# Kernel optimization log

Hardware: AMD Instinct MI355X
Metric: run time of the kernel (lower is better)

Reference implementation:

```python
import jax, jax.numpy as jnp
from jax import lax
import numpy as np

N = 4096      # graph nodes
K = 16        # sampled local-neighborhood size (2-hop proxy)
T = 16        # number of templates
NT = 16       # nodes per template
D = 128       # node feature dim
OUTER = 3     # proximal / mirror-descent iterations
INNER = 5     # sinkhorn iterations per outer step
EPS_REL = 0.1 # entropic reg relative to cost range
TINY = 1e-16


def setup_inputs() -> dict:
    key = jax.random.key(0)
    ks = jax.random.split(key, 8)
    x = jax.random.normal(ks[0], (N, D), jnp.float32)
    adj = (jax.random.uniform(ks[1], (N, N)) < 0.004).astype(jnp.float32)
    adj = jnp.maximum(adj, adj.T)
    neighbors = jax.random.randint(ks[2], (N, K), 0, N, dtype=jnp.int32)
    templates = (jax.random.randint(ks[3], (T, NT, NT), 0, 2).astype(jnp.float32)
                 + 0.01 * jax.random.normal(ks[4], (T, NT, NT), jnp.float32))
    templates_features = 0.0012 + 0.02 * jax.random.normal(ks[5], (T, NT, D), jnp.float32)
    q0 = jax.random.uniform(ks[6], (T, NT), jnp.float32)
    alpha0 = jnp.zeros((1,), jnp.float32)
    return {"x": x, "adj": adj, "neighbors": neighbors, "templates": templates,
            "templates_features": templates_features, "q0": q0, "alpha0": alpha0}


def _ltfgw(x, adj, neighbors, templates, templates_features, q0, alpha0):
    n, d = x.shape
    t, nt, _ = templates.shape
    k1 = neighbors.shape[1] + 1
    nb = jnp.concatenate([jnp.arange(n, dtype=neighbors.dtype)[:, None], neighbors], axis=1)  # [N,K1]
    Fi = x[nb]                                    # [N,K1,D] local node features
    C1 = adj[nb[:, :, None], nb[:, None, :]]      # [N,K1,K1] local structure
    C2 = templates                                # [T,NT,NT]
    alpha = jax.nn.sigmoid(alpha0[0])
    q = jax.nn.softmax(q0, axis=1)                # [T,NT] template node weights
    p = jnp.full((k1,), 1.0 / k1, x.dtype)        # uniform local weights
    # squared-euclidean feature cost M: [N,T,K1,NT]
    M = (jnp.sum(Fi**2, -1)[:, None, :, None]
         + jnp.sum(templates_features**2, -1)[None, :, None, :]
         - 2.0 * jnp.einsum('nkd,tmd->ntkm', Fi, templates_features))
    # constant part of squared-loss GW cost
    cC = (jnp.einsum('nij,j->ni', C1**2, p)[:, None, :, None]
          + jnp.einsum('tm,tlm->tl', q, C2**2)[None, :, None, :])
    G0 = jnp.broadcast_to(p[None, None, :, None] * q[None, :, None, :], (n, t, k1, nt))

    def outer_step(G, _):
        gw_grad = cC - 2.0 * jnp.einsum('nij,ntjm,tlm->ntil', C1, G, C2)
        grad = (1.0 - alpha) * M + alpha * gw_grad
        lo = jnp.min(grad, axis=(-2, -1), keepdims=True)
        hi = jnp.max(grad, axis=(-2, -1), keepdims=True)
        eps = EPS_REL * (hi - lo) + TINY
        Kmat = jnp.exp(-(grad - lo) / eps)        # per-(n,t) shift leaves plan invariant

        def sink(uv, _):
            u, v = uv
            u = p[None, None, :] / jnp.maximum(jnp.einsum('ntkm,ntm->ntk', Kmat, v), TINY)
            v = q[None] / jnp.maximum(jnp.einsum('ntkm,ntk->ntm', Kmat, u), TINY)
            return (u, v), None

        u0 = jnp.ones((n, t, k1), x.dtype)
        v0 = jnp.ones((n, t, nt), x.dtype)
        (u, v), _ = lax.scan(sink, (u0, v0), None, length=INNER)
        return u[..., None] * Kmat * v[..., None, :], None

    G, _ = lax.scan(outer_step, G0, None, length=OUTER)
    gw = cC - 2.0 * jnp.einsum('nij,ntjm,tlm->ntil', C1, G, C2)
    # fused GW distance of every node's local graph to every template: [N,T]
    return jnp.sum(((1.0 - alpha) * M + alpha * gw) * G, axis=(-2, -1))


def reference(x, adj, neighbors, templates, templates_features, q0, alpha0):
    return _ltfgw(x, adj, neighbors, templates, templates_features, q0, alpha0)
```

## Files before the change

### kernel.cpp

```cpp
#include <hip/hip_runtime.h>
#include <math.h>


#define NN 4096
#define KNB 16
#define K1 17
#define TSTR 296
#define TINYF 1e-16f

typedef const __attribute__((address_space(4))) float* c4fp;
typedef const __attribute__((address_space(4))) int*   c4ip;
__device__ __forceinline__ float sload(const float* p){ return *(c4fp)(unsigned long long)p; }
__device__ __forceinline__ int   sloadi(const int* p) { return *(c4ip)(unsigned long long)p; }

template<int CTRL>
__device__ __forceinline__ float dppmov(float x) {
  return __int_as_float(
      __builtin_amdgcn_update_dpp(0, __float_as_int(x), CTRL, 0xF, 0xF, true));
}
__device__ __forceinline__ float xor4v(float x) {
  return dppmov<0x1B>(dppmov<0x141>(x));
}
__device__ __forceinline__ float rsum16(float x) {
  x += dppmov<0xB1>(x); x += dppmov<0x4E>(x);
  x += xor4v(x);        x += dppmov<0x128>(x);
  return x;
}
__device__ __forceinline__ float rmin16(float x) {
  x = fminf(x, dppmov<0xB1>(x)); x = fminf(x, dppmov<0x4E>(x));
  x = fminf(x, xor4v(x));        x = fminf(x, dppmov<0x128>(x));
  return x;
}
__device__ __forceinline__ float rmax16(float x) {
  x = fmaxf(x, dppmov<0xB1>(x)); x = fmaxf(x, dppmov<0x4E>(x));
  x = fmaxf(x, xor4v(x));        x = fmaxf(x, dppmov<0x128>(x));
  return x;
}
__device__ __forceinline__ float rcpn(float x) {
  float r = __builtin_amdgcn_rcpf(x);
  return r * (2.f - x * r);
}

#define WSTEP(C, R) { g = dppmov<C>(g); acc = fmaf(g, c2reg[R], acc); }
#define WALK15() \
  WSTEP(0xB1,1)  WSTEP(0x1B,2)  WSTEP(0xB1,3)  WSTEP(0x141,4) \
  WSTEP(0xB1,5)  WSTEP(0x1B,6)  WSTEP(0xB1,7)  WSTEP(0x140,8) \
  WSTEP(0xB1,9)  WSTEP(0x1B,10) WSTEP(0xB1,11) WSTEP(0x141,12) \
  WSTEP(0xB1,13) WSTEP(0x1B,14) WSTEP(0xB1,15)

#define PG_GEMM  512
#define PG_PACK  (PG_GEMM + 1024)
#define PG_XSQ   (PG_PACK + 1024)
#define PG_SCAL  PG_XSQ
#define PG_TOT   (PG_SCAL + 1)

__global__ __launch_bounds__(256) void prep_combined(
    const float* __restrict__ x, const float* __restrict__ adj,
    const float* __restrict__ templates_, const float* __restrict__ tf,
    const float* __restrict__ q0, const float* __restrict__ alpha0,
    float* __restrict__ P, unsigned long long* __restrict__ pk,
    float* __restrict__ xsq, float* __restrict__ tfsq,
    float* __restrict__ qmat, float* __restrict__ cq,
    float* __restrict__ walpha) {
  __shared__ __align__(16) float smem[2 * 64 * 68];
  const int b = blockIdx.x, tid = threadIdx.x;

  if (b < PG_GEMM) {
    float (*As)[68] = (float (*)[68])smem;
    float (*Bs)[68] = (float (*)[68])(smem + 64*68);
    int tx = tid & 15, ty = tid >> 4;
    int r0 = (b & 127) * 32, c0 = (b >> 7) * 64;
    float acc[2][4] = {};
    for (int h = 0; h < 2; ++h) {
      __syncthreads();
#pragma unroll
      for (int q = 0; q < 2; ++q) {
        int f = tid + 256*q;
        int row = f >> 4, d4 = (f & 15) << 2;
        float4 a = *(const float4*)&x[(r0+row)*128 + h*64 + d4];
        As[d4+0][row]=a.x; As[d4+1][row]=a.y; As[d4+2][row]=a.z; As[d4+3][row]=a.w;
      }
#pragma unroll
      for (int q = 0; q < 4; ++q) {
        int f = tid + 256*q;
        int col = f >> 4, d4 = (f & 15) << 2;
        float4 bb = *(const float4*)&tf[(c0+col)*128 + h*64 + d4];
        Bs[d4+0][col]=bb.x; Bs[d4+1][col]=bb.y; Bs[d4+2][col]=bb.z; Bs[d4+3][col]=bb.w;
      }
      __syncthreads();
#pragma unroll
      for (int d = 0; d < 64; ++d) {
        float2 a = *(const float2*)&As[d][ty*2];
        float4 bb = *(const float4*)&Bs[d][tx*4];
        float av[2]={a.x,a.y}, bv[4]={bb.x,bb.y,bb.z,bb.w};
#pragma unroll
        for (int i = 0; i < 2; ++i)
#pragma unroll
          for (int j = 0; j < 4; ++j) acc[i][j] = fmaf(av[i], bv[j], acc[i][j]);
      }
    }
#pragma unroll
    for (int i = 0; i < 2; ++i) {
      float4 o; o.x=acc[i][0]; o.y=acc[i][1]; o.z=acc[i][2]; o.w=acc[i][3];
      *(float4*)&P[(r0 + ty*2 + i)*256 + c0 + tx*4] = o;
    }
    return;
  }

  if (b < PG_PACK) {
    int wave = (b - PG_GEMM)*4 + (tid >> 6);
    int lane = tid & 63;
#pragma unroll 4
    for (int it = 0; it < 64; ++it) {
      int w64 = wave + it*4096;
      float v = adj[(size_t)w64*64 + lane];
      unsigned long long m = __ballot(v != 0.f);
      if (lane == 0) pk[w64] = m;
    }
    return;
  }

  if (b < PG_XSQ) {
    int n = (b - PG_PACK)*4 + (tid >> 6), lane = tid & 63;
    float2 v = *(const float2*)&x[n*128 + lane*2];
    float s = fmaf(v.x, v.x, v.y*v.y);
    s += __shfl_xor(s,1); s += __shfl_xor(s,2);  s += __shfl_xor(s,4);
    s += __shfl_xor(s,8); s += __shfl_xor(s,16); s += __shfl_xor(s,32);
    if (lane == 0) xsq[n] = s;
    return;
  }

  {
    int t = tid >> 4, l = tid & 15;
    if (tid == 0) walpha[0] = 1.f / (1.f + expf(-alpha0[0]));
    float qr[16]; float mx = -3.0e38f;
#pragma unroll
    for (int m = 0; m < 16; ++m) { qr[m] = q0[t*16+m]; mx = fmaxf(mx, qr[m]); }
    float s = 0.f;
#pragma unroll
    for (int m = 0; m < 16; ++m) { qr[m] = expf(qr[m]-mx); s += qr[m]; }
    float inv = 1.f / s;
    qmat[tid] = qr[l] * inv;
    float c = 0.f;
#pragma unroll
    for (int m = 0; m < 16; ++m) {
      float c2 = templates_[t*256 + l*16 + m];
      c = fmaf(qr[m]*inv, c2*c2, c);
    }
    cq[tid] = c;
    float ts = 0.f;
#pragma unroll
    for (int dq = 0; dq < 32; ++dq) {
      float4 v = *(const float4*)&tf[tid*128 + dq*4];
      ts = fmaf(v.x,v.x,ts); ts = fmaf(v.y,v.y,ts);
      ts = fmaf(v.z,v.z,ts); ts = fmaf(v.w,v.w,ts);
    }
    tfsq[tid] = ts;
  }
}

__global__ __launch_bounds__(256, 2) void ltfgw_main(
    const float* __restrict__ P, const unsigned* __restrict__ pku,
    const float* __restrict__ xsq, const float* __restrict__ tfsq,
    const float* __restrict__ qmat, const float* __restrict__ cq,
    const float* __restrict__ walpha, const int* __restrict__ neighbors,
    const float* __restrict__ templates_, float* __restrict__ out) {
  __shared__ __align__(16) float Ksh[16 * TSTR];
  __shared__ __align__(16) float Ush[256];
  __shared__ __align__(16) float Vsh[256];
  __shared__ int rowm[20];

  const int tid = threadIdx.x;
  const int t = tid >> 4, l = tid & 15;
  const int n = blockIdx.x;

  const float alpha = sload(walpha);
  const float oma = 1.f - alpha;
  const float na2 = -2.f * alpha;

  int nbk[K1];
  nbk[0] = n;
#pragma unroll
  for (int k = 1; k < K1; ++k) nbk[k] = sloadi(neighbors + n*KNB + (k-1));

  if (tid < K1) {
    int row = (tid == 0) ? n : neighbors[n*KNB + tid - 1];
    const unsigned* prow = pku + row*128;
    unsigned m = 0;
#pragma unroll
    for (int j = 0; j < K1; ++j) {
      int col = nbk[j];
      unsigned w = prow[col >> 5];
      m |= ((w >> (col & 31)) & 1u) << j;
    }
    rowm[tid] = (int)m;
  }
  __syncthreads();
  int rmv[K1];
#pragma unroll
  for (int i = 0; i < K1; ++i) rmv[i] = rowm[i];

  const float tfsq_l = tfsq[tid];
  const float cq_l   = cq[tid];
  const float q_l    = qmat[tid];

  float Mcol[K1];
#pragma unroll
  for (int k = 0; k < K1; ++k) {
    float xs  = sload(xsq + nbk[k]);
    float cc1 = (float)__popc((unsigned)rmv[k]) * (1.f/17.f);
    float pv  = P[nbk[k]*256 + tid];
    Mcol[k] = oma * (xs + tfsq_l - 2.f*pv) + alpha * (cc1 + cq_l);
  }

  float c2reg[16];
#pragma unroll
  for (int r = 0; r < 16; ++r)
    c2reg[r] = na2 * templates_[t*256 + l*16 + (l ^ r)];

  float Gcol[K1];
#pragma unroll
  for (int j = 0; j < K1; ++j) Gcol[j] = (1.f/17.f) * q_l;

  const int tb = t * TSTR;
  float ur[16], u16 = 0.f, vm = 1.f;

#pragma unroll 1
  for (int outer = 0; outer < 3; ++outer) {
    float Kc[K1];
    float lo = 3.0e38f, hi = -3.0e38f;
#pragma unroll
    for (int i = 0; i < K1; ++i) {
      float gr = Mcol[i];
      int rmi = __builtin_amdgcn_readfirstlane(rmv[i]);
      if (rmi) {
        float s = 0.f;
#pragma unroll
        for (int j = 0; j < K1; ++j)
          if (rmi & (1 << j)) s += Gcol[j];
        float g = s, acc = s * c2reg[0];
        WALK15()
        gr += acc;
      }
      Kc[i] = gr;
      lo = fminf(lo, gr); hi = fmaxf(hi, gr);
    }
    lo = rmin16(lo); hi = rmax16(hi);
    float eps = 0.1f * (hi - lo) + TINYF;
    float sc = 1.4426950408889634f * __builtin_amdgcn_rcpf(eps);
#pragma unroll
    for (int i = 0; i < K1; ++i) {
      Kc[i] = __builtin_amdgcn_exp2f((lo - Kc[i]) * sc);
      Ksh[tb + i*17 + l] = Kc[i];
    }
    float Krow[16];
#pragma unroll
    for (int jq = 0; jq < 4; ++jq) {
      float4 v = *(const float4*)&Ksh[tb + l*17 + jq*4];
      Krow[jq*4+0]=v.x; Krow[jq*4+1]=v.y; Krow[jq*4+2]=v.z; Krow[jq*4+3]=v.w;
    }

    float vlane = 1.f;
    Vsh[tid] = 1.f;
#pragma unroll 1
    for (int it = 0; it < 5; ++it) {
      float vr[16];
#pragma unroll
      for (int q = 0; q < 4; ++q) {
        float4 v = *(const float4*)&Vsh[t*16 + q*4];
        vr[q*4+0]=v.x; vr[q*4+1]=v.y; vr[q*4+2]=v.z; vr[q*4+3]=v.w;
      }
      float w = 0.f;
#pragma unroll
      for (int j = 0; j < 16; ++j) w = fmaf(Krow[j], vr[j], w);
      float w16 = rsum16(Kc[16] * vlane);
      float um = (1.f/17.f) * rcpn(fmaxf(w,   TINYF));
      u16      = (1.f/17.f) * rcpn(fmaxf(w16, TINYF));
      Ush[tid] = um;
#pragma unroll
      for (int q = 0; q < 4; ++q) {
        float4 v = *(const float4*)&Ush[t*16 + q*4];
        ur[q*4+0]=v.x; ur[q*4+1]=v.y; ur[q*4+2]=v.z; ur[q*4+3]=v.w;
      }
      float sg = u16 * Kc[16];
#pragma unroll
      for (int k = 0; k < 16; ++k) sg = fmaf(ur[k], Kc[k], sg);
      vlane = q_l * rcpn(fmaxf(sg, TINYF));
      Vsh[tid] = vlane;
    }
    vm = vlane;
#pragma unroll
    for (int k = 0; k < 16; ++k) Gcol[k] = ur[k] * Kc[k] * vm;
    Gcol[16] = u16 * Kc[16] * vm;
  }

  float acc1 = 0.f;
#pragma unroll
  for (int i = 0; i < K1; ++i) acc1 = fmaf(Mcol[i], Gcol[i], acc1);
#pragma unroll
  for (int i = 0; i < K1; ++i) {
    int rmi = __builtin_amdgcn_readfirstlane(rmv[i]);
    if (rmi) {
      float s = 0.f;
#pragma unroll
      for (int j = 0; j < K1; ++j)
        if (rmi & (1 << j)) s += Gcol[j];
      float g = s, acc = s * c2reg[0];
      WALK15()
      acc1 = fmaf(acc, Gcol[i], acc1);
    }
  }
  float accout = rsum16(acc1);
  if (l == 0) out[n*16 + t] = accout;
}

extern "C" void kernel_launch(void* const* d_in, const int* in_sizes, int n_in,
                              void* d_out, int out_size, void* d_ws, size_t ws_size,
                              hipStream_t stream) {
  const float* x          = (const float*)d_in[0];
  const float* adj        = (const float*)d_in[1];
  const int*   neighbors  = (const int*)  d_in[2];
  const float* templates_ = (const float*)d_in[3];
  const float* tfeat      = (const float*)d_in[4];
  const float* q0         = (const float*)d_in[5];
  const float* alpha0     = (const float*)d_in[6];
  float* out = (float*)d_out;

  float* ws     = (float*)d_ws;
  float* P      = ws;
  float* xsq    = P + 4096*256;
  float* tfsq   = xsq + 4096;
  float* qmat   = tfsq + 256;
  float* cq     = qmat + 256;
  float* walpha = cq + 256;
  unsigned long long* pk = (unsigned long long*)(walpha + 8);

  hipLaunchKernelGGL(prep_combined, dim3(PG_TOT), dim3(256), 0, stream,
                     x, adj, templates_, tfeat, q0, alpha0,
                     P, pk, xsq, tfsq, qmat, cq, walpha);
  hipLaunchKernelGGL(ltfgw_main, dim3(4096), dim3(256), 0, stream,
                     P, (const unsigned*)pk, xsq, tfsq, qmat, cq, walpha,
                     neighbors, templates_, out);
}
```

Before: 195.4 us.

## Gather local adjacency bitmasks in prep kernel instead of packing full adjacency

The prep kernel no longer ballot-packs the whole 4096x4096 adjacency matrix into bits. Instead it gathers only the 17x17 local-structure entries per node directly from adj and writes per-node row bitmasks, which the main kernel reads as scalar loads. This drops a full 64MB adjacency read and removes a syncthreads plus the shared-memory handoff in the main kernel. Launch bounds are raised to 4 blocks per SIMD, which may force register spilling. Only 17 of every 64 lanes do the scattered gathers, so that part runs at low efficiency.

```diff
diff --git a/kernel.cpp b/kernel.cpp
--- a/kernel.cpp
+++ b/kernel.cpp
@@ -6,6 +6,7 @@
 #define KNB 16
 #define K1 17
 #define TSTR 296
+#define RBITS_STR 32
 #define TINYF 1e-16f
 
 typedef const __attribute__((address_space(4))) float* c4fp;
@@ -49,16 +50,17 @@
   WSTEP(0xB1,13) WSTEP(0x1B,14) WSTEP(0xB1,15)
 
 #define PG_GEMM  512
-#define PG_PACK  (PG_GEMM + 1024)
-#define PG_XSQ   (PG_PACK + 1024)
+#define PG_BITS  (PG_GEMM + 1024)
+#define PG_XSQ   (PG_BITS + 1024)
 #define PG_SCAL  PG_XSQ
 #define PG_TOT   (PG_SCAL + 1)
 
 __global__ __launch_bounds__(256) void prep_combined(
     const float* __restrict__ x, const float* __restrict__ adj,
-    const float* __restrict__ templates_, const float* __restrict__ tf,
-    const float* __restrict__ q0, const float* __restrict__ alpha0,
-    float* __restrict__ P, unsigned long long* __restrict__ pk,
+    const int* __restrict__ neighbors, const float* __restrict__ templates_,
+    const float* __restrict__ tf, const float* __restrict__ q0,
+    const float* __restrict__ alpha0,
+    float* __restrict__ P, int* __restrict__ rowbits,
     float* __restrict__ xsq, float* __restrict__ tfsq,
     float* __restrict__ qmat, float* __restrict__ cq,
     float* __restrict__ walpha) {
@@ -107,21 +109,28 @@
     return;
   }
 
-  if (b < PG_PACK) {
-    int wave = (b - PG_GEMM)*4 + (tid >> 6);
-    int lane = tid & 63;
-#pragma unroll 4
-    for (int it = 0; it < 64; ++it) {
-      int w64 = wave + it*4096;
-      float v = adj[(size_t)w64*64 + lane];
-      unsigned long long m = __ballot(v != 0.f);
-      if (lane == 0) pk[w64] = m;
+  if (b < PG_BITS) {
+    int g = b - PG_GEMM;
+    int sub = tid >> 6;
+    int row = tid & 63;
+    int n = g*4 + sub;
+    if (row < K1) {
+      int nbs[K1];
+      nbs[0] = n;
+#pragma unroll
+      for (int k = 1; k < K1; ++k) nbs[k] = neighbors[n*KNB + k - 1];
+      const float* arow = adj + (size_t)nbs[row]*NN;
+      unsigned m = 0;
+#pragma unroll
+      for (int j = 0; j < K1; ++j)
+        m |= (arow[nbs[j]] != 0.f ? 1u : 0u) << j;
+      rowbits[n*RBITS_STR + row] = (int)m;
     }
     return;
   }
 
   if (b < PG_XSQ) {
-    int n = (b - PG_PACK)*4 + (tid >> 6), lane = tid & 63;
+    int n = (b - PG_BITS)*4 + (tid >> 6), lane = tid & 63;
     float2 v = *(const float2*)&x[n*128 + lane*2];
     float s = fmaf(v.x, v.x, v.y*v.y);
     s += __shfl_xor(s,1); s += __shfl_xor(s,2);  s += __shfl_xor(s,4);
@@ -159,8 +168,8 @@
   }
 }
 
-__global__ __launch_bounds__(256, 2) void ltfgw_main(
-    const float* __restrict__ P, const unsigned* __restrict__ pku,
+__global__ __launch_bounds__(256, 4) void ltfgw_main(
+    const float* __restrict__ P, const int* __restrict__ rowbits,
     const float* __restrict__ xsq, const float* __restrict__ tfsq,
     const float* __restrict__ qmat, const float* __restrict__ cq,
     const float* __restrict__ walpha, const int* __restrict__ neighbors,
@@ -168,7 +177,6 @@
   __shared__ __align__(16) float Ksh[16 * TSTR];
   __shared__ __align__(16) float Ush[256];
   __shared__ __align__(16) float Vsh[256];
-  __shared__ int rowm[20];
 
   const int tid = threadIdx.x;
   const int t = tid >> 4, l = tid & 15;
@@ -183,22 +191,9 @@
 #pragma unroll
   for (int k = 1; k < K1; ++k) nbk[k] = sloadi(neighbors + n*KNB + (k-1));
 
-  if (tid < K1) {
-    int row = (tid == 0) ? n : neighbors[n*KNB + tid - 1];
-    const unsigned* prow = pku + row*128;
-    unsigned m = 0;
-#pragma unroll
-    for (int j = 0; j < K1; ++j) {
-      int col = nbk[j];
-      unsigned w = prow[col >> 5];
-      m |= ((w >> (col & 31)) & 1u) << j;
-    }
-    rowm[tid] = (int)m;
-  }
-  __syncthreads();
   int rmv[K1];
 #pragma unroll
-  for (int i = 0; i < K1; ++i) rmv[i] = rowm[i];
+  for (int i = 0; i < K1; ++i) rmv[i] = sloadi(rowbits + n*RBITS_STR + i);
 
   const float tfsq_l = tfsq[tid];
   const float cq_l   = cq[tid];
@@ -232,7 +227,7 @@
 #pragma unroll
     for (int i = 0; i < K1; ++i) {
       float gr = Mcol[i];
-      int rmi = __builtin_amdgcn_readfirstlane(rmv[i]);
+      int rmi = rmv[i];
       if (rmi) {
         float s = 0.f;
 #pragma unroll
@@ -299,7 +294,7 @@
   for (int i = 0; i < K1; ++i) acc1 = fmaf(Mcol[i], Gcol[i], acc1);
 #pragma unroll
   for (int i = 0; i < K1; ++i) {
-    int rmi = __builtin_amdgcn_readfirstlane(rmv[i]);
+    int rmi = rmv[i];
     if (rmi) {
       float s = 0.f;
 #pragma unroll
@@ -333,12 +328,12 @@
   float* qmat   = tfsq + 256;
   float* cq     = qmat + 256;
   float* walpha = cq + 256;
-  unsigned long long* pk = (unsigned long long*)(walpha + 8);
+  int*   rowbits= (int*)(walpha + 8);
 
   hipLaunchKernelGGL(prep_combined, dim3(PG_TOT), dim3(256), 0, stream,
-                     x, adj, templates_, tfeat, q0, alpha0,
-                     P, pk, xsq, tfsq, qmat, cq, walpha);
+                     x, adj, neighbors, templates_, tfeat, q0, alpha0,
+                     P, rowbits, xsq, tfsq, qmat, cq, walpha);
   hipLaunchKernelGGL(ltfgw_main, dim3(4096), dim3(256), 0, stream,
-                     P, (const unsigned*)pk, xsq, tfsq, qmat, cq, walpha,
-                     neighbors, templates_, out);
-}
+                     P, rowbits, xsq, tfsq, qmat, cq, walpha, neighbors,
+                     templates_, out);
+}
```

New measurement: 203.5 us. 1.04x slower.
